# Optimization experiments

Measured on AMD Instinct MI355X. Metric: run time of the kernel, lower is better.

Reference implementation:

```python
import jax, jax.numpy as jnp
import numpy as np

B, D_IN, H, V, T = 8192, 2048, 1024, 6, 6  # batch, enc input, hidden, total_vocab, max_length
TAU = 1.0

def setup_inputs() -> dict:
    key = jax.random.key(0)
    ks = jax.random.split(key, 16)
    s = 0.02
    return {
        "x": jax.random.normal(ks[0], (B, D_IN), jnp.float32),
        "u_noise": jax.random.uniform(ks[1], (T, B, V), jnp.float32),
        "W_enc": jax.random.normal(ks[2], (D_IN, H), jnp.float32) * s,
        "b_enc": jnp.zeros((H,), jnp.float32),
        "start_embed": jax.random.normal(ks[3], (H,), jnp.float32) * 0.01,
        "W_tok": jax.random.normal(ks[4], (V, H), jnp.float32) * s,
        "b_tok": jnp.zeros((H,), jnp.float32),
        "Wz": jax.random.normal(ks[5], (2 * H, H), jnp.float32) * s,
        "bz": jnp.zeros((H,), jnp.float32),
        "Wr": jax.random.normal(ks[6], (2 * H, H), jnp.float32) * s,
        "br": jnp.zeros((H,), jnp.float32),
        "Wh": jax.random.normal(ks[7], (2 * H, H), jnp.float32) * s,
        "bh": jnp.zeros((H,), jnp.float32),
        "W_out": jax.random.normal(ks[8], (H, V), jnp.float32) * s,
        "b_out": jnp.zeros((V,), jnp.float32),
    }

def reference(x, u_noise, W_enc, b_enc, start_embed, W_tok, b_tok,
              Wz, bz, Wr, br, Wh, bh, W_out, b_out):
    eps = 1e-10
    # uniform -> Gumbel(0,1) noise, precomputed per step: (T, B, V)
    g_all = -jnp.log(-jnp.log(u_noise + eps) + eps)
    h0 = x @ W_enc + b_enc                                   # encoder: (B, H)
    batch = x.shape[0]
    prev0 = jnp.broadcast_to(start_embed, (batch, start_embed.shape[0]))
    rc0 = jnp.ones((batch, 1), x.dtype)                      # running continue mask
    nt0 = jnp.zeros((batch,), x.dtype)                       # differentiable token count

    def step(carry, g):
        h, prev, rc, nt = carry
        nt = nt + rc[:, 0]
        comb = jnp.concatenate([prev, h], axis=-1)           # (B, 2H)
        z = jax.nn.sigmoid(comb @ Wz + bz)
        r = jax.nn.sigmoid(comb @ Wr + br)
        comb_r = jnp.concatenate([prev, r * h], axis=-1)
        h_tilde = jnp.tanh(comb_r @ Wh + bh)
        h = (1 - z) * h + z * h_tilde                        # GRU update
        logits = h @ W_out + b_out                           # (B, V)
        # hard gumbel-softmax with straight-through estimator
        y_soft = jax.nn.softmax((logits + g) / TAU, axis=-1)
        y_hard = jax.nn.one_hot(jnp.argmax(y_soft, axis=-1), logits.shape[-1],
                                dtype=logits.dtype)
        token = y_hard - jax.lax.stop_gradient(y_soft) + y_soft
        masked = token * rc                                  # zero out after STOP
        rc = rc * (1 - token[:, -1:])                        # STOP is last symbol
        prev = token @ W_tok + b_tok
        return (h, prev, rc, nt), (masked, logits)

    (_, _, _, n_tokens), (masked_seq, logits_seq) = jax.lax.scan(
        step, (h0, prev0, rc0, nt0), g_all)
    # (T, B, V) -> (B, T*V) message
    message = jnp.transpose(masked_seq, (1, 0, 2)).reshape(batch, -1)
    return message, logits_seq, n_tokens
```

## Files before the change

kernel.cpp:

```cpp
#include <hip/hip_runtime.h>
#include <math.h>

#define B_ 8192
#define DIN_ 2048
#define H_ 1024
#define V_ 6
#define T_ 6

typedef short bf16x8 __attribute__((ext_vector_type(8)));
typedef float f32x4 __attribute__((ext_vector_type(4)));

__device__ __forceinline__ unsigned short f32_bf16(float f) {
    unsigned u = __float_as_uint(f);
    u += 0x7FFFu + ((u >> 16) & 1u);
    return (unsigned short)(u >> 16);
}
__device__ __forceinline__ float bf16_f32(unsigned short h) {
    return __uint_as_float(((unsigned)h) << 16);
}

#define GLL16(g, l) __builtin_amdgcn_global_load_lds(                       \
        (const __attribute__((address_space(1))) void*)(g),                  \
        (__attribute__((address_space(3))) void*)(l), 16, 0, 0)

__global__ __launch_bounds__(256) void conv_w(const float* __restrict__ W,
        unsigned short* __restrict__ hi, unsigned short* __restrict__ lo)
{
    const int t = blockIdx.x * 256 + threadIdx.x;
    const int n = t & 1023;
    const int kb = t >> 10;
    unsigned hq[4], lq[4];
#pragma unroll
    for (int p = 0; p < 4; ++p) {
        const float v0 = W[(size_t)(kb * 8 + 2 * p) * 1024 + n];
        const float v1 = W[(size_t)(kb * 8 + 2 * p + 1) * 1024 + n];
        const unsigned short h0 = f32_bf16(v0), h1 = f32_bf16(v1);
        const unsigned short l0 = f32_bf16(v0 - bf16_f32(h0));
        const unsigned short l1 = f32_bf16(v1 - bf16_f32(h1));
        hq[p] = (unsigned)h0 | ((unsigned)h1 << 16);
        lq[p] = (unsigned)l0 | ((unsigned)l1 << 16);
    }
    const size_t c = ((size_t)(n >> 4) * 256 + kb) * 128 + (size_t)(n & 15) * 8;
    *(uint4*)(hi + c) = make_uint4(hq[0], hq[1], hq[2], hq[3]);
    *(uint4*)(lo + c) = make_uint4(lq[0], lq[1], lq[2], lq[3]);
}

__global__ __launch_bounds__(256) void conv_wb(const float* __restrict__ W,
        unsigned short* __restrict__ hi, unsigned short* __restrict__ lo)
{
    const int t = blockIdx.x * 256 + threadIdx.x;
    const int n = t & 1023;
    const int kb = t >> 10;
    unsigned hq[4], lq[4];
#pragma unroll
    for (int p = 0; p < 4; ++p) {
        const float v0 = W[(size_t)(1024 + kb * 8 + 2 * p) * 1024 + n];
        const float v1 = W[(size_t)(1024 + kb * 8 + 2 * p + 1) * 1024 + n];
        const unsigned short h0 = f32_bf16(v0), h1 = f32_bf16(v1);
        const unsigned short l0 = f32_bf16(v0 - bf16_f32(h0));
        const unsigned short l1 = f32_bf16(v1 - bf16_f32(h1));
        hq[p] = (unsigned)h0 | ((unsigned)h1 << 16);
        lq[p] = (unsigned)l0 | ((unsigned)l1 << 16);
    }
    const size_t c = ((size_t)(n >> 4) * 128 + kb) * 128 + (size_t)(n & 15) * 8;
    *(uint4*)(hi + c) = make_uint4(hq[0], hq[1], hq[2], hq[3]);
    *(uint4*)(lo + c) = make_uint4(lq[0], lq[1], lq[2], lq[3]);
}

__global__ __launch_bounds__(256) void conv_x(const float* __restrict__ X,
        unsigned short* __restrict__ hi, unsigned short* __restrict__ lo)
{
    const size_t t = (size_t)blockIdx.x * 256 + threadIdx.x;
    const int kb = (int)(t & 255);
    const int m = (int)(t >> 8);
    const float4 f0 = *(const float4*)(X + (size_t)m * 2048 + kb * 8);
    const float4 f1 = *(const float4*)(X + (size_t)m * 2048 + kb * 8 + 4);
    const float v[8] = {f0.x, f0.y, f0.z, f0.w, f1.x, f1.y, f1.z, f1.w};
    unsigned hq[4], lq[4];
#pragma unroll
    for (int p = 0; p < 4; ++p) {
        const unsigned short h0 = f32_bf16(v[2 * p]);
        const unsigned short h1 = f32_bf16(v[2 * p + 1]);
        const unsigned short l0 = f32_bf16(v[2 * p] - bf16_f32(h0));
        const unsigned short l1 = f32_bf16(v[2 * p + 1] - bf16_f32(h1));
        hq[p] = (unsigned)h0 | ((unsigned)h1 << 16);
        lq[p] = (unsigned)l0 | ((unsigned)l1 << 16);
    }
    const size_t c = ((size_t)(m >> 4) * 256 + kb) * 128 + (size_t)(m & 15) * 8;
    *(uint4*)(hi + c) = make_uint4(hq[0], hq[1], hq[2], hq[3]);
    *(uint4*)(lo + c) = make_uint4(lq[0], lq[1], lq[2], lq[3]);
}

__global__ __launch_bounds__(256) void prep_tables(
        const float* __restrict__ Wz, const float* __restrict__ Wr,
        const float* __restrict__ Wh,
        const float* __restrict__ bz, const float* __restrict__ br,
        const float* __restrict__ bh,
        const float* __restrict__ Wt, const float* __restrict__ bt,
        const float* __restrict__ se,
        float* __restrict__ Pz, float* __restrict__ Pr, float* __restrict__ Ph)
{
    __shared__ float emb[7][1024];
    const int tid = threadIdx.x;
    for (int i = tid; i < 7 * 1024; i += 256) {
        const int r = i >> 10, k = i & 1023;
        emb[r][k] = (r < 6) ? (Wt[(size_t)r * 1024 + k] + bt[k]) : se[k];
    }
    __syncthreads();
    const float* W = (blockIdx.y == 0) ? Wz : ((blockIdx.y == 1) ? Wr : Wh);
    const float* bb = (blockIdx.y == 0) ? bz : ((blockIdx.y == 1) ? br : bh);
    float* P = (blockIdx.y == 0) ? Pz : ((blockIdx.y == 1) ? Pr : Ph);
    const int n = blockIdx.x * 256 + tid;
    float acc[7] = {0.f, 0.f, 0.f, 0.f, 0.f, 0.f, 0.f};
    for (int k = 0; k < 1024; ++k) {
        const float wv = W[(size_t)k * 1024 + n];
#pragma unroll
        for (int r = 0; r < 7; ++r) acc[r] = fmaf(emb[r][k], wv, acc[r]);
    }
    const float bvv = bb[n];
#pragma unroll
    for (int r = 0; r < 7; ++r) P[(size_t)r * 1024 + n] = acc[r] + bvv;
}

__global__ __launch_bounds__(256) void init_misc(
        int* __restrict__ tokidx, float* __restrict__ rc, float* __restrict__ nt)
{
    const int t = blockIdx.x * 256 + threadIdx.x;
    tokidx[t] = 6;
    rc[t] = 1.0f;
    nt[t] = 0.0f;
}

__global__ __launch_bounds__(512, 2)
void gemm256(
    const unsigned short* __restrict__ A_hi, const unsigned short* __restrict__ A_lo,
    const unsigned short* __restrict__ B0_hi, const unsigned short* __restrict__ B0_lo,
    const unsigned short* __restrict__ B1_hi, const unsigned short* __restrict__ B1_lo,
    const float* __restrict__ P0, const float* __restrict__ P1,
    const int* __restrict__ tokidx,
    const float* __restrict__ zbuf, float* __restrict__ hbuf,
    float* __restrict__ outf,
    unsigned short* __restrict__ ophi, unsigned short* __restrict__ oplo,
    int nkb, int mode)
{
    __shared__ unsigned short lds[3 * 24576];

    const int tid = threadIdx.x;
    const int lane = tid & 63;
    const int w = tid >> 6;

    const int NX = gridDim.x;
    const int lin = blockIdx.y * NX + blockIdx.x;
    const int xcd = lin & 7;
    const int idx = lin >> 3;
    int bx = idx % NX;
    const int by = xcd * 4 + idx / NX;

    const unsigned short* Bhi = B0_hi;
    const unsigned short* Blo = B0_lo;
    const float* Pm = P0;
    int isR = 0;
    if (mode == 1 && bx >= 8) { bx -= 8; Bhi = B1_hi; Blo = B1_lo; Pm = P1; isR = 1; }

    const int m0 = by * 256;
    const int n0 = bx * 128;
    const int mg0 = by * 16;
    const int ng0 = bx * 8;

    const int pa = w >> 2;
    const int ga0 = (w & 3) * 4;
    const int nb0 = (w & 3) * 2;
    const unsigned short* Asrc = pa ? A_lo : A_hi;
    const unsigned short* Bsrc = pa ? Blo : Bhi;

    f32x4 acc[4][4];
#pragma unroll
    for (int i = 0; i < 4; ++i)
#pragma unroll
        for (int j = 0; j < 4; ++j) acc[i][j] = (f32x4){0.f, 0.f, 0.f, 0.f};

    const int wr = w & 3;
    const int wc = w >> 2;
    const int fq = lane >> 4;
    const int fm = lane & 15;
    const int nsteps = nkb >> 2;

#define STAGE(tt, bb) do {                                                     \
    unsigned short* db_ = lds + (bb) * 24576;                                  \
    const size_t kb0_ = (size_t)(tt) * 4;                                      \
    _Pragma("unroll")                                                          \
    for (int q = 0; q < 4; ++q) {                                              \
        const size_t so = ((size_t)(mg0 + ga0 + q) * nkb + kb0_) * 128 + lane * 8; \
        GLL16(Asrc + so, db_ + pa * 8192 + (ga0 + q) * 512 + lane * 8);        \
    }                                                                          \
    _Pragma("unroll")                                                          \
    for (int q = 0; q < 2; ++q) {                                              \
        const size_t so = ((size_t)(ng0 + nb0 + q) * nkb + kb0_) * 128 + lane * 8; \
        GLL16(Bsrc + so, db_ + 16384 + pa * 4096 + (nb0 + q) * 512 + lane * 8);\
    }                                                                          \
} while (0)

#define COMPUTE(bb) do {                                                       \
    const unsigned short* db_ = lds + (bb) * 24576;                            \
    bf16x8 bh4_[4], bl4_[4];                                                   \
    _Pragma("unroll")                                                          \
    for (int j = 0; j < 4; ++j) {                                              \
        const int rb = 16384 + (wc * 4 + j) * 512 + fq * 128 + fm * 8;         \
        bh4_[j] = *(const bf16x8*)(db_ + rb);                                  \
        bl4_[j] = *(const bf16x8*)(db_ + rb + 4096);                           \
    }                                                                          \
    _Pragma("unroll")                                                          \
    for (int i = 0; i < 4; ++i) {                                              \
        const int ra = (wr * 4 + i) * 512 + fq * 128 + fm * 8;                 \
        const bf16x8 ah = *(const bf16x8*)(db_ + ra);                          \
        const bf16x8 al = *(const bf16x8*)(db_ + ra + 8192);                   \
        __builtin_amdgcn_s_setprio(1);                                         \
        _Pragma("unroll")                                                      \
        for (int j = 0; j < 4; ++j) {                                          \
            acc[i][j] = __builtin_amdgcn_mfma_f32_16x16x32_bf16(ah, bh4_[j], acc[i][j], 0, 0, 0); \
            acc[i][j] = __builtin_amdgcn_mfma_f32_16x16x32_bf16(ah, bl4_[j], acc[i][j], 0, 0, 0); \
            acc[i][j] = __builtin_amdgcn_mfma_f32_16x16x32_bf16(al, bh4_[j], acc[i][j], 0, 0, 0); \
        }                                                                      \
        __builtin_amdgcn_s_setprio(0);                                         \
    }                                                                          \
} while (0)

    STAGE(0, 0);
    STAGE(1, 1);

    int cb = 0;
#pragma unroll 1
    for (int t = 0; t < nsteps - 2; ++t) {
        const int sb = (cb >= 1) ? (cb - 1) : 2;
        STAGE(t + 2, sb);
        asm volatile("s_waitcnt vmcnt(12)" ::: "memory");
        __builtin_amdgcn_s_barrier();
        __builtin_amdgcn_sched_barrier(0);
        COMPUTE(cb);
        asm volatile("s_waitcnt lgkmcnt(0)" ::: "memory");
        __builtin_amdgcn_s_barrier();
        __builtin_amdgcn_sched_barrier(0);
        cb = (cb == 2) ? 0 : cb + 1;
    }
    asm volatile("s_waitcnt vmcnt(6)" ::: "memory");
    __builtin_amdgcn_s_barrier();
    __builtin_amdgcn_sched_barrier(0);
    COMPUTE(cb);
    asm volatile("s_waitcnt lgkmcnt(0)" ::: "memory");
    __builtin_amdgcn_s_barrier();
    __builtin_amdgcn_sched_barrier(0);
    cb = (cb == 2) ? 0 : cb + 1;
    asm volatile("s_waitcnt vmcnt(0)" ::: "memory");
    __builtin_amdgcn_s_barrier();
    __builtin_amdgcn_sched_barrier(0);
    COMPUTE(cb);

#undef STAGE
#undef COMPUTE

#pragma unroll
    for (int i = 0; i < 4; ++i) {
        int toks[4];
#pragma unroll
        for (int r = 0; r < 4; ++r) {
            const int row = m0 + wr * 64 + i * 16 + fq * 4 + r;
            toks[r] = tokidx ? tokidx[row] : 0;
        }
#pragma unroll
        for (int j = 0; j < 4; ++j) {
            const int col = n0 + wc * 64 + j * 16 + fm;
#pragma unroll
            for (int r = 0; r < 4; ++r) {
                const int row = m0 + wr * 64 + i * 16 + fq * 4 + r;
                const float v = acc[i][j][r] + Pm[(size_t)toks[r] * 1024 + col];
                const size_t off = (size_t)row * 1024 + col;
                const size_t pc = ((size_t)(row >> 4) * 128 + (col >> 3)) * 128
                                  + (size_t)(row & 15) * 8 + (col & 7);
                if (mode == 0) {
                    hbuf[off] = v;
                    const unsigned short hv = f32_bf16(v);
                    ophi[pc] = hv;
                    oplo[pc] = f32_bf16(v - bf16_f32(hv));
                } else if (mode == 1) {
                    const float sg = 1.0f / (1.0f + expf(-v));
                    if (!isR) {
                        outf[off] = sg;
                    } else {
                        const float rh = sg * hbuf[off];
                        const unsigned short hv = f32_bf16(rh);
                        ophi[pc] = hv;
                        oplo[pc] = f32_bf16(rh - bf16_f32(hv));
                    }
                } else {
                    const float tv = tanhf(v);
                    const float zv = zbuf[off];
                    const float hn = (1.0f - zv) * hbuf[off] + zv * tv;
                    hbuf[off] = hn;
                    const unsigned short hv = f32_bf16(hn);
                    ophi[pc] = hv;
                    oplo[pc] = f32_bf16(hn - bf16_f32(hv));
                }
            }
        }
    }
}

__global__ __launch_bounds__(256)
void step_tok(const float* __restrict__ h,
              const float* __restrict__ W_out, const float* __restrict__ b_out,
              const float* __restrict__ u,
              float* __restrict__ rc, float* __restrict__ nt,
              int* __restrict__ tokidx,
              float* __restrict__ out_msg, float* __restrict__ out_logits,
              float* __restrict__ out_nt, int t)
{
    const int lane = threadIdx.x & 63;
    const int wv = threadIdx.x >> 6;
    const int b = blockIdx.x * 4 + wv;

    const float* hr = h + (size_t)b * H_;
    float s[6] = {0.f, 0.f, 0.f, 0.f, 0.f, 0.f};
#pragma unroll
    for (int i = 0; i < 4; ++i) {
        const int k0 = i * 256 + lane * 4;
        const float4 hv = *(const float4*)(hr + k0);
        const float he[4] = {hv.x, hv.y, hv.z, hv.w};
#pragma unroll
        for (int e = 0; e < 4; ++e) {
            const float* wp = W_out + (size_t)(k0 + e) * V_;
            const float xv = he[e];
#pragma unroll
            for (int v = 0; v < 6; ++v) s[v] = fmaf(xv, wp[v], s[v]);
        }
    }
#pragma unroll
    for (int m = 1; m < 64; m <<= 1) {
#pragma unroll
        for (int v = 0; v < 6; ++v) s[v] += __shfl_xor(s[v], m, 64);
    }

    float lg[6];
#pragma unroll
    for (int v = 0; v < 6; ++v) lg[v] = s[v] + b_out[v];

    const float* ub = u + (size_t)b * V_;
    const float eps = 1e-10f;
    float aa[6];
#pragma unroll
    for (int v = 0; v < 6; ++v) {
        const float g = -logf(-logf(ub[v] + eps) + eps);
        aa[v] = lg[v] + g;
    }
    int tok = 0;
    float best = aa[0];
#pragma unroll
    for (int v = 1; v < 6; ++v)
        if (aa[v] > best) { best = aa[v]; tok = v; }

    if (lane == 0) {
        const float rco = rc[b];
#pragma unroll
        for (int v = 0; v < 6; ++v) out_logits[(size_t)b * 6 + v] = lg[v];
#pragma unroll
        for (int v = 0; v < 6; ++v)
            out_msg[(size_t)b * 36 + t * 6 + v] = (v == tok) ? rco : 0.0f;
        const float ntn = nt[b] + rco;
        nt[b] = ntn;
        out_nt[b] = ntn;
        rc[b] = (tok == 5) ? 0.0f : rco;
        tokidx[b] = tok;
    }
}

extern "C" void kernel_launch(void* const* d_in, const int* in_sizes, int n_in,
                              void* d_out, int out_size, void* d_ws, size_t ws_size,
                              hipStream_t stream)
{
    (void)in_sizes; (void)n_in; (void)out_size; (void)ws_size;
    const float* x       = (const float*)d_in[0];
    const float* u_noise = (const float*)d_in[1];
    const float* W_enc   = (const float*)d_in[2];
    const float* b_enc   = (const float*)d_in[3];
    const float* start_e = (const float*)d_in[4];
    const float* W_tok   = (const float*)d_in[5];
    const float* b_tok   = (const float*)d_in[6];
    const float* Wz      = (const float*)d_in[7];
    const float* bz      = (const float*)d_in[8];
    const float* Wr      = (const float*)d_in[9];
    const float* br      = (const float*)d_in[10];
    const float* Wh      = (const float*)d_in[11];
    const float* bh      = (const float*)d_in[12];
    const float* W_out   = (const float*)d_in[13];
    const float* b_out   = (const float*)d_in[14];

    float* out = (float*)d_out;
    float* out_msg = out;
    float* out_logits = out + (size_t)B_ * T_ * V_;
    float* out_nt = out_logits + (size_t)T_ * B_ * V_;

    char* wsb = (char*)d_ws;
    const size_t MB = 1024 * 1024;
    unsigned short* wzb_hi = (unsigned short*)(wsb + 0 * MB);
    unsigned short* wzb_lo = (unsigned short*)(wsb + 2 * MB);
    unsigned short* wrb_hi = (unsigned short*)(wsb + 4 * MB);
    unsigned short* wrb_lo = (unsigned short*)(wsb + 6 * MB);
    unsigned short* whb_hi = (unsigned short*)(wsb + 8 * MB);
    unsigned short* whb_lo = (unsigned short*)(wsb + 10 * MB);
    unsigned short* we_hi  = (unsigned short*)(wsb + 12 * MB);
    unsigned short* we_lo  = (unsigned short*)(wsb + 16 * MB);
    unsigned short* x_hi   = (unsigned short*)(wsb + 20 * MB);
    unsigned short* x_lo   = (unsigned short*)(wsb + 52 * MB);
    float*  zbuf  = (float*)(wsb + 20 * MB);
    unsigned short* rh_hi  = (unsigned short*)(wsb + 52 * MB);
    unsigned short* rh_lo  = (unsigned short*)(wsb + 68 * MB);
    float*  hbuf  = (float*)(wsb + 84 * MB);
    unsigned short* h_hi   = (unsigned short*)(wsb + 116 * MB);
    unsigned short* h_lo   = (unsigned short*)(wsb + 132 * MB);
    float* Pz = (float*)(wsb + 148 * MB);
    float* Pr = Pz + 7 * 1024;
    float* Ph = Pr + 7 * 1024;
    int* tokidx = (int*)(Ph + 7 * 1024);
    float* rcb = (float*)(tokidx + B_);
    float* ntb = rcb + B_;

    conv_wb<<<512, 256, 0, stream>>>(Wz, wzb_hi, wzb_lo);
    conv_wb<<<512, 256, 0, stream>>>(Wr, wrb_hi, wrb_lo);
    conv_wb<<<512, 256, 0, stream>>>(Wh, whb_hi, whb_lo);
    conv_w<<<1024, 256, 0, stream>>>(W_enc, we_hi, we_lo);
    conv_x<<<8192, 256, 0, stream>>>(x, x_hi, x_lo);
    prep_tables<<<dim3(4, 3), 256, 0, stream>>>(Wz, Wr, Wh, bz, br, bh,
                                                W_tok, b_tok, start_e, Pz, Pr, Ph);
    init_misc<<<32, 256, 0, stream>>>(tokidx, rcb, ntb);

    gemm256<<<dim3(8, 32), 512, 0, stream>>>(
        x_hi, x_lo, we_hi, we_lo, nullptr, nullptr,
        b_enc, nullptr, nullptr,
        nullptr, hbuf, nullptr, h_hi, h_lo, 256, 0);

    for (int t = 0; t < T_; ++t) {
        gemm256<<<dim3(16, 32), 512, 0, stream>>>(
            h_hi, h_lo, wzb_hi, wzb_lo, wrb_hi, wrb_lo,
            Pz, Pr, tokidx,
            nullptr, hbuf, zbuf, rh_hi, rh_lo, 128, 1);
        gemm256<<<dim3(8, 32), 512, 0, stream>>>(
            rh_hi, rh_lo, whb_hi, whb_lo, nullptr, nullptr,
            Ph, nullptr, tokidx,
            zbuf, hbuf, nullptr, h_hi, h_lo, 128, 2);
        step_tok<<<B_ / 4, 256, 0, stream>>>(
            hbuf, W_out, b_out, u_noise + (size_t)t * B_ * V_,
            rcb, ntb, tokidx, out_msg,
            out_logits + (size_t)t * B_ * V_, out_nt, t);
    }
}
```

Measured before the change: 1.876 ms.

## Interleave global-to-LDS staging with MFMA sub-tiles in a ping-pong GEMM schedule

Splits each K-step of the 3-term bf16-split GEMM into four sub-phases, each issuing a few global_load_lds ops and one row-group of LDS reads and then 12 MFMAs, separated by barriers. The aim is to spread memory issue across the compute phase instead of front-loading it, so loads and MFMAs overlap more evenly. The cost is many more workgroup barriers per iteration, plus a reworked vmcnt wait accounting whose correctness depends on the staging order.

```diff
diff --git a/kernel.cpp b/kernel.cpp
--- a/kernel.cpp
+++ b/kernel.cpp
@@ -185,78 +185,108 @@
     const int fm = lane & 15;
     const int nsteps = nkb >> 2;
 
-#define STAGE(tt, bb) do {                                                     \
-    unsigned short* db_ = lds + (bb) * 24576;                                  \
-    const size_t kb0_ = (size_t)(tt) * 4;                                      \
+#define STG_A2(tt_, dst_, q0_) do {                                            \
     _Pragma("unroll")                                                          \
-    for (int q = 0; q < 4; ++q) {                                              \
-        const size_t so = ((size_t)(mg0 + ga0 + q) * nkb + kb0_) * 128 + lane * 8; \
-        GLL16(Asrc + so, db_ + pa * 8192 + (ga0 + q) * 512 + lane * 8);        \
+    for (int q = (q0_); q < (q0_) + 2; ++q) {                                  \
+        const size_t so = ((size_t)(mg0 + ga0 + q) * nkb + (size_t)(tt_) * 4) * 128 + lane * 8; \
+        GLL16(Asrc + so, (dst_) + pa * 8192 + (ga0 + q) * 512 + lane * 8);     \
     }                                                                          \
+} while (0)
+
+#define STG_B2(tt_, dst_) do {                                                 \
     _Pragma("unroll")                                                          \
     for (int q = 0; q < 2; ++q) {                                              \
-        const size_t so = ((size_t)(ng0 + nb0 + q) * nkb + kb0_) * 128 + lane * 8; \
-        GLL16(Bsrc + so, db_ + 16384 + pa * 4096 + (nb0 + q) * 512 + lane * 8);\
+        const size_t so = ((size_t)(ng0 + nb0 + q) * nkb + (size_t)(tt_) * 4) * 128 + lane * 8; \
+        GLL16(Bsrc + so, (dst_) + 16384 + pa * 4096 + (nb0 + q) * 512 + lane * 8); \
     }                                                                          \
 } while (0)
 
-#define COMPUTE(bb) do {                                                       \
-    const unsigned short* db_ = lds + (bb) * 24576;                            \
-    bf16x8 bh4_[4], bl4_[4];                                                   \
+#define BAR() do { __builtin_amdgcn_s_barrier();                               \
+                   __builtin_amdgcn_sched_barrier(0); } while (0)
+#define LGKM0() do { asm volatile("s_waitcnt lgkmcnt(0)" ::: "memory");        \
+                     __builtin_amdgcn_sched_barrier(0); } while (0)
+
+#define DS_B(db_) do {                                                         \
     _Pragma("unroll")                                                          \
     for (int j = 0; j < 4; ++j) {                                              \
         const int rb = 16384 + (wc * 4 + j) * 512 + fq * 128 + fm * 8;         \
-        bh4_[j] = *(const bf16x8*)(db_ + rb);                                  \
-        bl4_[j] = *(const bf16x8*)(db_ + rb + 4096);                           \
+        bh4_[j] = *(const bf16x8*)((db_) + rb);                                \
+        bl4_[j] = *(const bf16x8*)((db_) + rb + 4096);                         \
     }                                                                          \
+} while (0)
+
+#define DS_A(db_, i_) do {                                                     \
+    const int ra = (wr * 4 + (i_)) * 512 + fq * 128 + fm * 8;                  \
+    ah_ = *(const bf16x8*)((db_) + ra);                                        \
+    al_ = *(const bf16x8*)((db_) + ra + 8192);                                 \
+} while (0)
+
+#define MFMA12(i_) do {                                                        \
+    __builtin_amdgcn_s_setprio(1);                                             \
     _Pragma("unroll")                                                          \
-    for (int i = 0; i < 4; ++i) {                                              \
-        const int ra = (wr * 4 + i) * 512 + fq * 128 + fm * 8;                 \
-        const bf16x8 ah = *(const bf16x8*)(db_ + ra);                          \
-        const bf16x8 al = *(const bf16x8*)(db_ + ra + 8192);                   \
-        __builtin_amdgcn_s_setprio(1);                                         \
-        _Pragma("unroll")                                                      \
-        for (int j = 0; j < 4; ++j) {                                          \
-            acc[i][j] = __builtin_amdgcn_mfma_f32_16x16x32_bf16(ah, bh4_[j], acc[i][j], 0, 0, 0); \
-            acc[i][j] = __builtin_amdgcn_mfma_f32_16x16x32_bf16(ah, bl4_[j], acc[i][j], 0, 0, 0); \
-            acc[i][j] = __builtin_amdgcn_mfma_f32_16x16x32_bf16(al, bh4_[j], acc[i][j], 0, 0, 0); \
-        }                                                                      \
-        __builtin_amdgcn_s_setprio(0);                                         \
+    for (int j = 0; j < 4; ++j) {                                              \
+        acc[i_][j] = __builtin_amdgcn_mfma_f32_16x16x32_bf16(ah_, bh4_[j], acc[i_][j], 0, 0, 0); \
+        acc[i_][j] = __builtin_amdgcn_mfma_f32_16x16x32_bf16(ah_, bl4_[j], acc[i_][j], 0, 0, 0); \
+        acc[i_][j] = __builtin_amdgcn_mfma_f32_16x16x32_bf16(al_, bh4_[j], acc[i_][j], 0, 0, 0); \
     }                                                                          \
-} while (0)
-
-    STAGE(0, 0);
-    STAGE(1, 1);
+    __builtin_amdgcn_s_setprio(0);                                             \
+} while (0)
+
+#define TILE_BODY(cbuf_, sbuf_, tt_, DOSTG_, EW_) do {                         \
+    const unsigned short* db_ = lds + (cbuf_) * 24576;                         \
+    unsigned short* dsb_ = lds + (sbuf_) * 24576;                              \
+    (void)dsb_;                                                                \
+    bf16x8 bh4_[4], bl4_[4], ah_, al_;                                         \
+                                                                  \
+    DS_B(db_); DS_A(db_, 0);                                                   \
+    if (DOSTG_) STG_A2(tt_, dsb_, 0);                                          \
+    BAR(); LGKM0(); MFMA12(0); BAR();                                          \
+                                                                  \
+    DS_A(db_, 1);                                                              \
+    if (DOSTG_) STG_A2(tt_, dsb_, 2);                                          \
+    BAR(); LGKM0(); MFMA12(1); BAR();                                          \
+                                                                  \
+    DS_A(db_, 2);                                                              \
+    if (DOSTG_) STG_B2(tt_, dsb_);                                             \
+    BAR(); LGKM0(); MFMA12(2); BAR();                                          \
+                                                                  \
+    DS_A(db_, 3);                                                              \
+    BAR(); LGKM0(); MFMA12(3);                                                 \
+    if ((EW_) == 6) { asm volatile("s_waitcnt vmcnt(6)" ::: "memory"); }       \
+    else if ((EW_) == 0) { asm volatile("s_waitcnt vmcnt(0)" ::: "memory"); }  \
+    __builtin_amdgcn_sched_barrier(0);                                         \
+    BAR();                                                                     \
+} while (0)
+
+    STG_A2(0, lds, 0); STG_A2(0, lds, 2); STG_B2(0, lds);
+    {
+        unsigned short* dsb_ = lds + 24576;
+        STG_A2(1, dsb_, 0); STG_A2(1, dsb_, 2); STG_B2(1, dsb_);
+    }
+    asm volatile("s_waitcnt vmcnt(6)" ::: "memory");
+    __builtin_amdgcn_sched_barrier(0);
+    __builtin_amdgcn_s_barrier();
+    __builtin_amdgcn_sched_barrier(0);
 
     int cb = 0;
 #pragma unroll 1
     for (int t = 0; t < nsteps - 2; ++t) {
-        const int sb = (cb >= 1) ? (cb - 1) : 2;
-        STAGE(t + 2, sb);
-        asm volatile("s_waitcnt vmcnt(12)" ::: "memory");
-        __builtin_amdgcn_s_barrier();
-        __builtin_amdgcn_sched_barrier(0);
-        COMPUTE(cb);
-        asm volatile("s_waitcnt lgkmcnt(0)" ::: "memory");
-        __builtin_amdgcn_s_barrier();
-        __builtin_amdgcn_sched_barrier(0);
+        const int sbn = (cb >= 1) ? (cb - 1) : 2;
+        TILE_BODY(cb, sbn, t + 2, 1, 6);
         cb = (cb == 2) ? 0 : cb + 1;
     }
-    asm volatile("s_waitcnt vmcnt(6)" ::: "memory");
-    __builtin_amdgcn_s_barrier();
-    __builtin_amdgcn_sched_barrier(0);
-    COMPUTE(cb);
-    asm volatile("s_waitcnt lgkmcnt(0)" ::: "memory");
-    __builtin_amdgcn_s_barrier();
-    __builtin_amdgcn_sched_barrier(0);
+    TILE_BODY(cb, 0, 0, 0, 0);
     cb = (cb == 2) ? 0 : cb + 1;
-    asm volatile("s_waitcnt vmcnt(0)" ::: "memory");
-    __builtin_amdgcn_s_barrier();
-    __builtin_amdgcn_sched_barrier(0);
-    COMPUTE(cb);
-
-#undef STAGE
-#undef COMPUTE
+    TILE_BODY(cb, 0, 0, 0, -1);
+
+#undef TILE_BODY
+#undef MFMA12
+#undef DS_A
+#undef DS_B
+#undef LGKM0
+#undef BAR
+#undef STG_B2
+#undef STG_A2
 
 #pragma unroll
     for (int i = 0; i < 4; ++i) {
```

New measurement: 1.807 ms. -3.7%, faster.
